# Performance work log

Measured on AMD Instinct MI355X. Metric: run time of the kernel, lower is better.

The kernel has to match this reference:

```python
import jax, jax.numpy as jnp
import numpy as np

TOP_K = 10        # top_k init arg
GAMMA = 0.7       # gamma init arg: weight on user's own prediction
TEMP = 0.5        # temperature for softmax over neighbor similarities
NEG_INF = -1e9    # used to exclude self from top-k (finite for bf16/fp16 safety)


def setup_inputs() -> dict:
    key = jax.random.key(0)
    k1, k2, k3 = jax.random.split(key, 3)
    N_USERS, N_ITEMS, BATCH = 8192, 4096, 2048
    # binary-ish user-item interaction matrix (sparse implicit feedback)
    full_user_vectors = (jax.random.uniform(k1, (N_USERS, N_ITEMS)) < 0.05).astype(jnp.float32)
    # diffusion-model denoised predictions for the batch
    predictions = jax.random.normal(k2, (BATCH, N_ITEMS), dtype=jnp.float32)
    batch_indices = jax.random.randint(k3, (BATCH,), 0, N_USERS)
    return {"predictions": predictions,
            "full_user_vectors": full_user_vectors,
            "batch_indices": batch_indices}


def reference(predictions, full_user_vectors, batch_indices):
    eps = 1e-8
    # cosine similarity matrix over all users: normalize rows, then GEMM
    norms = jnp.linalg.norm(full_user_vectors, axis=1, keepdims=True)
    normed = full_user_vectors / jnp.maximum(norms, eps)          # [N, I]
    sim = normed @ normed.T                                        # [N, N]
    n = sim.shape[0]
    diag = jnp.arange(n)
    sim = sim.at[diag, diag].set(NEG_INF)                          # exclude self
    # top-k similar users per user
    topk_sims, topk_idx = jax.lax.top_k(sim, TOP_K)                # [N, k]
    # gather for the batch
    b_sims = topk_sims[batch_indices]                              # [B, k]
    b_idx = topk_idx[batch_indices]                                # [B, k]
    weights = jax.nn.softmax(b_sims / TEMP, axis=-1)               # [B, k]
    neighbor_vecs = full_user_vectors[b_idx]                       # [B, k, I]
    agg = jnp.einsum('bk,bki->bi', weights, neighbor_vecs)         # [B, I]
    # gamma-weighted blend of own prediction and neighbor aggregate
    return GAMMA * predictions + (1.0 - GAMMA) * agg
```

## Files before the change

### kernel.cpp

```cpp
#include <hip/hip_runtime.h>
#include <hip/hip_bf16.h>

typedef int i32x4 __attribute__((ext_vector_type(4)));
typedef float f32x4 __attribute__((ext_vector_type(4)));
typedef unsigned char uchar8 __attribute__((ext_vector_type(8)));
typedef unsigned char uchar4v __attribute__((ext_vector_type(4)));
typedef float float4v __attribute__((ext_vector_type(4)));

#define N_USERS 8192
#define N_ITEMS 4096
#define BATCH   2048
#define TOPK    10

__device__ __forceinline__ void gload16(const unsigned char* src, char* dst) {
    __builtin_amdgcn_global_load_lds(
        (const __attribute__((address_space(1))) unsigned int*)src,
        (__attribute__((address_space(3))) unsigned int*)dst, 16, 0, 0);
}

__global__ __launch_bounds__(256)
void convert_rows(const float* __restrict__ A, unsigned char* __restrict__ Ai8,
                  float* __restrict__ invn) {
    __shared__ float wsum[4];
    const int row  = blockIdx.x;
    const int tid  = threadIdx.x;
    const int wave = tid >> 6;
    const int lane = tid & 63;
    const float* src = A + (size_t)row * N_ITEMS;
    unsigned char* dst = Ai8 + (size_t)row * N_ITEMS;
    float s = 0.f;
#pragma unroll
    for (int i = 0; i < 4; ++i) {
        const int col = tid * 4 + i * 1024;
        float4v v = *(const float4v*)(src + col);
        uchar4v o;
#pragma unroll
        for (int j = 0; j < 4; ++j) {
            o[j] = (unsigned char)(v[j] != 0.f);
            s += v[j];
        }
        *(uchar4v*)(dst + col) = o;
    }
#pragma unroll
    for (int o = 32; o > 0; o >>= 1) s += __shfl_down(s, o);
    if (lane == 0) wsum[wave] = s;
    __syncthreads();
    if (tid == 0) {
        float t = wsum[0] + wsum[1] + wsum[2] + wsum[3];
        invn[row] = (t > 0.f) ? (1.0f / sqrtf(t)) : 0.f;
    }
}

#define BAR_MID() do { __builtin_amdgcn_s_barrier(); \
    asm volatile("s_waitcnt lgkmcnt(0)" ::: "memory"); \
    __builtin_amdgcn_sched_barrier(0); \
    __builtin_amdgcn_s_setprio(1); } while (0)

#define BAR_END() do { __builtin_amdgcn_s_setprio(0); \
    __builtin_amdgcn_sched_barrier(0); \
    __builtin_amdgcn_s_barrier(); } while (0)

#define BAR_END_VM4() do { __builtin_amdgcn_s_setprio(0); \
    __builtin_amdgcn_sched_barrier(0); \
    asm volatile("s_waitcnt vmcnt(4)" ::: "memory"); \
    __builtin_amdgcn_sched_barrier(0); \
    __builtin_amdgcn_s_barrier(); } while (0)

#define BAR_END_VM0() do { __builtin_amdgcn_s_setprio(0); \
    __builtin_amdgcn_sched_barrier(0); \
    asm volatile("s_waitcnt vmcnt(0)" ::: "memory"); \
    __builtin_amdgcn_sched_barrier(0); \
    __builtin_amdgcn_s_barrier(); } while (0)

#define RD_A4(dst, bo, mofs) \
  _Pragma("unroll") for (int m_ = 0; m_ < 4; ++m_) { \
    dst[m_*2+0] = *(const i32x4*)(lds + (bo) + arowb + (m_+(mofs))*2048 + cb0); \
    dst[m_*2+1] = *(const i32x4*)(lds + (bo) + arowb + (m_+(mofs))*2048 + cb1); }

#define RD_B2(dst, bo, nofs) \
  _Pragma("unroll") for (int n_ = 0; n_ < 2; ++n_) { \
    dst[n_*2+0] = *(const i32x4*)(lds + (bo) + browb + (n_+(nofs))*2048 + cb0); \
    dst[n_*2+1] = *(const i32x4*)(lds + (bo) + browb + (n_+(nofs))*2048 + cb1); }

#define MMA4x2(afr, bfr, mofs, nofs) \
  _Pragma("unroll") for (int m_ = 0; m_ < 4; ++m_) \
  _Pragma("unroll") for (int n_ = 0; n_ < 2; ++n_) { \
    acc[m_+(mofs)][n_+(nofs)] = __builtin_amdgcn_mfma_i32_16x16x64_i8( \
        afr[m_*2+0], bfr[n_*2+0], acc[m_+(mofs)][n_+(nofs)], 0, 0, 0); \
    acc[m_+(mofs)][n_+(nofs)] = __builtin_amdgcn_mfma_i32_16x16x64_i8( \
        afr[m_*2+1], bfr[n_*2+1], acc[m_+(mofs)][n_+(nofs)], 0, 0, 0); }

#define WINDOW(bo, S0, S1, S2, S3, ENDW) do { \
    RD_A4(af,  bo, 0); RD_B2(bf01, bo, 0); S0; \
    BAR_MID(); MMA4x2(af,  bf01, 0, 0); BAR_END(); \
    RD_B2(bf23, bo, 2); S1; \
    BAR_MID(); MMA4x2(af,  bf23, 0, 2); BAR_END(); \
    RD_A4(af2, bo, 4); S2; \
    BAR_MID(); MMA4x2(af2, bf01, 4, 0); BAR_END(); \
    S3; \
    BAR_MID(); MMA4x2(af2, bf23, 4, 2); ENDW; \
} while (0)

__global__ __launch_bounds__(512, 2)
void sim_gemm8(const unsigned char* __restrict__ A,
               const int* __restrict__ bidx,
               const float* __restrict__ invn,
               float* __restrict__ sim) {
    __shared__ char lds[131072];

    const int tid  = threadIdx.x;
    const int w    = tid >> 6;
    const int lane = tid & 63;
    const int m0   = blockIdx.y * 256;
    const int n0   = blockIdx.x * 256;
    const int wr = w >> 2, wc = w & 3;

    const int fr = lane & 15, ks = lane >> 4;
    const int swz = (fr & 7) << 4;
    const int cb0 = (ks * 16) ^ swz;
    const int cb1 = (ks * 16 + 64) ^ swz;
    const int arowb = wr * 16384 + fr * 128;
    const int browb = 32768 + (wc >> 1) * 16384 + ((wc & 1) * 64 + fr) * 128;

    const int sr = lane >> 3;
    const int swzcolB = ((lane & 7) ^ sr) * 16;
    const unsigned char* pA[4];
    const unsigned char* pB[4];
#pragma unroll
    for (int g = 0; g < 4; ++g) {
        const int row = g * 64 + w * 8 + sr;
        pA[g] = A + (size_t)bidx[m0 + row] * N_ITEMS + swzcolB;
        pB[g] = A + (size_t)(n0 + row) * N_ITEMS + swzcolB;
    }

    i32x4 acc[8][4] = {};
    i32x4 af[8], af2[8], bf01[4], bf23[4];

#define STA(U, h) do { \
    char* d_ = lds + (((U) & 1) * 65536) + (h) * 16384 + w * 1024; \
    const int k0_ = (U) * 128; \
    gload16(pA[(h)*2+0] + k0_, d_); \
    gload16(pA[(h)*2+1] + k0_, d_ + 8192); } while (0)

#define STB(U, h) do { \
    char* d_ = lds + (((U) & 1) * 65536) + 32768 + (h) * 16384 + w * 1024; \
    const int k0_ = (U) * 128; \
    gload16(pB[(h)*2+0] + k0_, d_); \
    gload16(pB[(h)*2+1] + k0_, d_ + 8192); } while (0)

    STA(0, 0); STA(0, 1); STB(0, 0); STB(0, 1); STA(1, 0); STA(1, 1);
    asm volatile("s_waitcnt vmcnt(4)" ::: "memory");
    __builtin_amdgcn_s_barrier();

    for (int i = 0; i < 15; ++i) {
        const int t1 = 2 * i + 1, t2 = 2 * i + 2, t3 = 2 * i + 3;
        WINDOW(0,     STB(t1, 0), STB(t1, 1), STA(t2, 0), STA(t2, 1), BAR_END_VM4());
        WINDOW(65536, STB(t2, 0), STB(t2, 1), STA(t3, 0), STA(t3, 1), BAR_END_VM4());
    }
    WINDOW(0,     STB(31, 0), STB(31, 1), (void)0, (void)0, BAR_END_VM0());
    WINDOW(65536, (void)0, (void)0, (void)0, (void)0, BAR_END());

    const int crow_base = m0 + wr * 128 + ks * 4;
    const int ccol_base = n0 + wc * 64 + fr;
#pragma unroll
    for (int mf = 0; mf < 8; ++mf) {
#pragma unroll
        for (int j = 0; j < 4; ++j) {
            const int b  = crow_base + mf * 16 + j;
            const int ub = bidx[b];
            const float inb = invn[ub];
            float* rp = sim + (size_t)b * N_USERS;
#pragma unroll
            for (int nf = 0; nf < 4; ++nf) {
                const int nn = ccol_base + nf * 16;
                float v = (float)acc[mf][nf][j] * inb * invn[nn];
                if (nn == ub) v = -1e9f;
                rp[nn] = v;
            }
        }
    }
#undef STA
#undef STB
}

__global__ __launch_bounds__(256)
void topk_blend(const float* __restrict__ sim,
                const unsigned char* __restrict__ Ai8,
                const float* __restrict__ pred,
                float* __restrict__ out) {
    __shared__ float srow[N_USERS];
    __shared__ float bvs[256];
    __shared__ int   bis[256];

    const int b    = blockIdx.x;
    const int tid  = threadIdx.x;
    const int lane = tid & 63;

    const float* sr = sim + (size_t)b * N_USERS;
    float bv = -1e30f; int bi = 0x7fffffff;
#pragma unroll
    for (int k = 0; k < 8; ++k) {
        const int slot = tid + k * 256;
        float4v v = ((const float4v*)sr)[slot];
        *(float4v*)(srow + slot * 4) = v;
#pragma unroll
        for (int j = 0; j < 4; ++j)
            if (v[j] > bv) { bv = v[j]; bi = slot * 4 + j; }
    }
    bvs[tid] = bv; bis[tid] = bi;
    __syncthreads();

    float topv[TOPK]; int topi[TOPK];
#pragma unroll
    for (int it = 0; it < TOPK; ++it) {
        float fv = bvs[lane]; int fi = bis[lane];
#pragma unroll
        for (int g = 1; g < 4; ++g) {
            float v2 = bvs[lane + g * 64]; int i2 = bis[lane + g * 64];
            if (v2 > fv || (v2 == fv && i2 < fi)) { fv = v2; fi = i2; }
        }
#pragma unroll
        for (int o = 1; o < 64; o <<= 1) {
            float ov = __shfl_xor(fv, o);
            int   oi = __shfl_xor(fi, o);
            if (ov > fv || (ov == fv && oi < fi)) { fv = ov; fi = oi; }
        }
        topv[it] = fv; topi[it] = fi;
        __syncthreads();
        if (tid == ((fi >> 2) & 255)) {
            srow[fi] = -1e30f;
            float nb = -1e30f; int ni = 0x7fffffff;
#pragma unroll
            for (int k = 0; k < 8; ++k) {
                const int slot = tid + k * 256;
                float4v v = *(const float4v*)(srow + slot * 4);
#pragma unroll
                for (int j = 0; j < 4; ++j)
                    if (v[j] > nb) { nb = v[j]; ni = slot * 4 + j; }
            }
            bvs[tid] = nb; bis[tid] = ni;
        }
        __syncthreads();
    }

    float w[TOPK];
    float mx = -1e30f;
#pragma unroll
    for (int k = 0; k < TOPK; ++k) mx = fmaxf(mx, topv[k]);
    float sumw = 0.f;
#pragma unroll
    for (int k = 0; k < TOPK; ++k) {
        w[k] = __expf((topv[k] - mx) * 2.0f);
        sumw += w[k];
    }
    const float scl = 0.3f / sumw;
#pragma unroll
    for (int k = 0; k < TOPK; ++k) w[k] *= scl;

    const float* pr = pred + (size_t)b * N_ITEMS;
    float*       po = out  + (size_t)b * N_ITEMS;
#pragma unroll
    for (int h = 0; h < 2; ++h) {
        const int col = h * 2048 + tid * 8;
        float4v p0 = *(const float4v*)(pr + col);
        float4v p1 = *(const float4v*)(pr + col + 4);
        float agg[8];
#pragma unroll
        for (int j = 0; j < 8; ++j) agg[j] = 0.f;
#pragma unroll
        for (int k = 0; k < TOPK; ++k) {
            uchar8 nv = *(const uchar8*)(Ai8 + (size_t)topi[k] * N_ITEMS + col);
#pragma unroll
            for (int j = 0; j < 8; ++j) agg[j] += w[k] * (float)nv[j];
        }
        float4v o0, o1;
#pragma unroll
        for (int j = 0; j < 4; ++j) {
            o0[j] = 0.7f * p0[j] + agg[j];
            o1[j] = 0.7f * p1[j] + agg[j + 4];
        }
        *(float4v*)(po + col)     = o0;
        *(float4v*)(po + col + 4) = o1;
    }
}

extern "C" void kernel_launch(void* const* d_in, const int* in_sizes, int n_in,
                              void* d_out, int out_size, void* d_ws, size_t ws_size,
                              hipStream_t stream) {
    const float* pred = (const float*)d_in[0];
    const float* A    = (const float*)d_in[1];
    const int*   bidx = (const int*)d_in[2];
    float*       out  = (float*)d_out;

    unsigned char* Ai8  = (unsigned char*)d_ws;
    float*         invn = (float*)((char*)d_ws + (size_t)N_USERS * N_ITEMS);
    float*         sim  = (float*)((char*)d_ws + (size_t)N_USERS * N_ITEMS + 65536);

    convert_rows<<<N_USERS, 256, 0, stream>>>(A, Ai8, invn);
    sim_gemm8<<<dim3(N_USERS / 256, BATCH / 256), 512, 0, stream>>>(Ai8, bidx, invn, sim);
    topk_blend<<<BATCH, 256, 0, stream>>>(sim, Ai8, pred, out);
}
```

Before: 139.4 us.

## Split top-k into per-wave register selection with packed 64-bit keys, then blend

The fused top-k+blend kernel is split in two. A wave-per-row select kernel keeps 32 per-chunk maxima in registers as packed (value, index) 64-bit keys, extracts the top 10 with wave shuffles, and rescans only one chunk from global memory per step. This removes the 32KB LDS row copy and the block-wide barriers of the previous version. A separate blend kernel reads the keys back, which adds one launch and a small intermediate buffer in the workspace.

```diff
diff --git a/kernel.cpp b/kernel.cpp
--- a/kernel.cpp
+++ b/kernel.cpp
@@ -2,10 +2,10 @@
 #include <hip/hip_bf16.h>
 
 typedef int i32x4 __attribute__((ext_vector_type(4)));
-typedef float f32x4 __attribute__((ext_vector_type(4)));
 typedef unsigned char uchar8 __attribute__((ext_vector_type(8)));
 typedef unsigned char uchar4v __attribute__((ext_vector_type(4)));
 typedef float float4v __attribute__((ext_vector_type(4)));
+typedef unsigned long long u64;
 
 #define N_USERS 8192
 #define N_ITEMS 4096
@@ -183,74 +183,89 @@
 #undef STB
 }
 
+__device__ __forceinline__ u64 packkey(float f, int idx) {
+    unsigned u = __float_as_uint(f);
+    u = ((int)u < 0) ? ~u : (u | 0x80000000u);
+    return ((u64)u << 32) | (unsigned)(~idx);
+}
+
 __global__ __launch_bounds__(256)
-void topk_blend(const float* __restrict__ sim,
-                const unsigned char* __restrict__ Ai8,
-                const float* __restrict__ pred,
-                float* __restrict__ out) {
-    __shared__ float srow[N_USERS];
-    __shared__ float bvs[256];
-    __shared__ int   bis[256];
-
-    const int b    = blockIdx.x;
-    const int tid  = threadIdx.x;
-    const int lane = tid & 63;
-
-    const float* sr = sim + (size_t)b * N_USERS;
-    float bv = -1e30f; int bi = 0x7fffffff;
-#pragma unroll
-    for (int k = 0; k < 8; ++k) {
-        const int slot = tid + k * 256;
-        float4v v = ((const float4v*)sr)[slot];
-        *(float4v*)(srow + slot * 4) = v;
-#pragma unroll
-        for (int j = 0; j < 4; ++j)
-            if (v[j] > bv) { bv = v[j]; bi = slot * 4 + j; }
-    }
-    bvs[tid] = bv; bis[tid] = bi;
-    __syncthreads();
-
-    float topv[TOPK]; int topi[TOPK];
-#pragma unroll
+void select10(const float* __restrict__ sim, u64* __restrict__ keys) {
+    const int wave = threadIdx.x >> 6;
+    const int lane = threadIdx.x & 63;
+    const int r    = blockIdx.x * 4 + wave;
+    const float* sr = sim + (size_t)r * N_USERS;
+
+    u64 cmax[32];
+#pragma unroll
+    for (int k = 0; k < 32; ++k) {
+        const int slot = k * 64 + lane;
+        float4v f = *(const float4v*)(sr + slot * 4);
+        u64 a = packkey(f[0], slot * 4 + 0);
+        u64 b = packkey(f[1], slot * 4 + 1);
+        u64 c = packkey(f[2], slot * 4 + 2);
+        u64 d = packkey(f[3], slot * 4 + 3);
+        u64 ab = a > b ? a : b, cd = c > d ? c : d;
+        cmax[k] = ab > cd ? ab : cd;
+    }
+    u64 lmax = cmax[0];
+#pragma unroll
+    for (int k = 1; k < 32; ++k) lmax = cmax[k] > lmax ? cmax[k] : lmax;
+
+    u64 myout = 0;
+#pragma unroll 1
     for (int it = 0; it < TOPK; ++it) {
-        float fv = bvs[lane]; int fi = bis[lane];
-#pragma unroll
-        for (int g = 1; g < 4; ++g) {
-            float v2 = bvs[lane + g * 64]; int i2 = bis[lane + g * 64];
-            if (v2 > fv || (v2 == fv && i2 < fi)) { fv = v2; fi = i2; }
-        }
+        u64 wkey = lmax;
 #pragma unroll
         for (int o = 1; o < 64; o <<= 1) {
-            float ov = __shfl_xor(fv, o);
-            int   oi = __shfl_xor(fi, o);
-            if (ov > fv || (ov == fv && oi < fi)) { fv = ov; fi = oi; }
-        }
-        topv[it] = fv; topi[it] = fi;
-        __syncthreads();
-        if (tid == ((fi >> 2) & 255)) {
-            srow[fi] = -1e30f;
-            float nb = -1e30f; int ni = 0x7fffffff;
-#pragma unroll
-            for (int k = 0; k < 8; ++k) {
-                const int slot = tid + k * 256;
-                float4v v = *(const float4v*)(srow + slot * 4);
-#pragma unroll
-                for (int j = 0; j < 4; ++j)
-                    if (v[j] > nb) { nb = v[j]; ni = slot * 4 + j; }
+            u64 ok = __shfl_xor(wkey, o);
+            if (ok > wkey) wkey = ok;
+        }
+        if (lane == it) myout = wkey;
+        const int widx = (int)(~(unsigned)wkey);
+        const int slot = widx >> 2;
+        if (lane == (slot & 63)) {
+            const int kc = slot >> 6;
+            float4v f = *(const float4v*)(sr + slot * 4);
+            u64 m = 0;
+#pragma unroll
+            for (int j = 0; j < 4; ++j) {
+                u64 kj = packkey(f[j], slot * 4 + j);
+                if (kj < wkey && kj > m) m = kj;
             }
-            bvs[tid] = nb; bis[tid] = ni;
-        }
-        __syncthreads();
-    }
-
-    float w[TOPK];
+#pragma unroll
+            for (int k = 0; k < 32; ++k) if (k == kc) cmax[k] = m;
+            lmax = cmax[0];
+#pragma unroll
+            for (int k = 1; k < 32; ++k) lmax = cmax[k] > lmax ? cmax[k] : lmax;
+        }
+    }
+    if (lane < TOPK) keys[(size_t)r * TOPK + lane] = myout;
+}
+
+__global__ __launch_bounds__(256)
+void blend(const u64* __restrict__ keys,
+           const unsigned char* __restrict__ Ai8,
+           const float* __restrict__ pred,
+           float* __restrict__ out) {
+    const int b   = blockIdx.x;
+    const int tid = threadIdx.x;
+
+    float w[TOPK]; int nid[TOPK];
     float mx = -1e30f;
 #pragma unroll
-    for (int k = 0; k < TOPK; ++k) mx = fmaxf(mx, topv[k]);
+    for (int k = 0; k < TOPK; ++k) {
+        u64 kk = keys[(size_t)b * TOPK + k];
+        unsigned hi = (unsigned)(kk >> 32);
+        unsigned bits = (hi & 0x80000000u) ? (hi ^ 0x80000000u) : ~hi;
+        w[k] = __uint_as_float(bits);
+        nid[k] = (int)(~(unsigned)kk);
+        mx = fmaxf(mx, w[k]);
+    }
     float sumw = 0.f;
 #pragma unroll
     for (int k = 0; k < TOPK; ++k) {
-        w[k] = __expf((topv[k] - mx) * 2.0f);
+        w[k] = __expf((w[k] - mx) * 2.0f);
         sumw += w[k];
     }
     const float scl = 0.3f / sumw;
@@ -269,7 +284,7 @@
         for (int j = 0; j < 8; ++j) agg[j] = 0.f;
 #pragma unroll
         for (int k = 0; k < TOPK; ++k) {
-            uchar8 nv = *(const uchar8*)(Ai8 + (size_t)topi[k] * N_ITEMS + col);
+            uchar8 nv = *(const uchar8*)(Ai8 + (size_t)nid[k] * N_ITEMS + col);
 #pragma unroll
             for (int j = 0; j < 8; ++j) agg[j] += w[k] * (float)nv[j];
         }
@@ -295,8 +310,11 @@
     unsigned char* Ai8  = (unsigned char*)d_ws;
     float*         invn = (float*)((char*)d_ws + (size_t)N_USERS * N_ITEMS);
     float*         sim  = (float*)((char*)d_ws + (size_t)N_USERS * N_ITEMS + 65536);
+    u64*           keys = (u64*)((char*)d_ws + (size_t)N_USERS * N_ITEMS + 65536
+                                 + (size_t)BATCH * N_USERS * sizeof(float));
 
     convert_rows<<<N_USERS, 256, 0, stream>>>(A, Ai8, invn);
     sim_gemm8<<<dim3(N_USERS / 256, BATCH / 256), 512, 0, stream>>>(Ai8, bidx, invn, sim);
-    topk_blend<<<BATCH, 256, 0, stream>>>(sim, Ai8, pred, out);
-}
+    select10<<<BATCH / 4, 256, 0, stream>>>(sim, keys);
+    blend<<<BATCH, 256, 0, stream>>>(keys, Ai8, pred, out);
+}
```

Measured after the change: 140.5 us. About the same (+0.8%).
